# Kernel optimization log

Measured on AMD Instinct MI355X. Metric: run time of the kernel, lower is better.

The kernel has to match this reference:

```python
import jax, jax.numpy as jnp
import numpy as np


def setup_inputs() -> dict:
    key = jax.random.key(0)
    B, S, I, H, O = 32, 2048, 128, 512, 128
    ks = jax.random.split(key, 24)
    sc = 0.05
    d = {
        "x": jax.random.normal(ks[0], (B, S, I), jnp.float32),
        "h0": jnp.zeros((B, 2, H), jnp.float32),
        "l0_wxz": jax.random.normal(ks[1], (H, I)) * sc,
        "l0_bxz": jax.random.normal(ks[2], (H,)) * sc,
        "l0_whz": jax.random.normal(ks[3], (H, H)) * sc,
        "l0_wxr": jax.random.normal(ks[4], (H, I)) * sc,
        "l0_bxr": jax.random.normal(ks[5], (H,)) * sc,
        "l0_whr": jax.random.normal(ks[6], (H, H)) * sc,
        "l0_wxg": jax.random.normal(ks[7], (H, I)) * sc,
        "l0_bxg": jax.random.normal(ks[8], (H,)) * sc,
        "l0_whg": jax.random.normal(ks[9], (H, H)) * sc,
        "l1_wxz": jax.random.normal(ks[10], (H, H)) * sc,
        "l1_bxz": jax.random.normal(ks[11], (H,)) * sc,
        "l1_whz": jax.random.normal(ks[12], (H, H)) * sc,
        "l1_wxr": jax.random.normal(ks[13], (H, H)) * sc,
        "l1_bxr": jax.random.normal(ks[14], (H,)) * sc,
        "l1_whr": jax.random.normal(ks[15], (H, H)) * sc,
        "l1_wxg": jax.random.normal(ks[16], (H, H)) * sc,
        "l1_bxg": jax.random.normal(ks[17], (H,)) * sc,
        "l1_whg": jax.random.normal(ks[18], (H, H)) * sc,
        "wy": jax.random.normal(ks[19], (O, H)) * sc,
        "by": jax.random.normal(ks[20], (O,)) * sc,
    }
    return d


def _gru_cell(xt, h, wxz, bxz, whz, wxr, bxr, whr, wxg, bxg, whg):
    # z = sigmoid(Wxz x + bxz + Whz h); r = sigmoid(...); g = tanh(Wxg x + bxg + Whg (r*h))
    z = jax.nn.sigmoid(xt @ wxz.T + bxz + h @ whz.T)
    r = jax.nn.sigmoid(xt @ wxr.T + bxr + h @ whr.T)
    g = jnp.tanh(xt @ wxg.T + bxg + (r * h) @ whg.T)
    return z * h + (1.0 - z) * g


def reference(x, h0,
              l0_wxz, l0_bxz, l0_whz, l0_wxr, l0_bxr, l0_whr, l0_wxg, l0_bxg, l0_whg,
              l1_wxz, l1_bxz, l1_whz, l1_wxr, l1_bxr, l1_whr, l1_wxg, l1_bxg, l1_whg,
              wy, by):
    p0 = (l0_wxz, l0_bxz, l0_whz, l0_wxr, l0_bxr, l0_whr, l0_wxg, l0_bxg, l0_whg)
    p1 = (l1_wxz, l1_bxz, l1_whz, l1_wxr, l1_bxr, l1_whr, l1_wxg, l1_bxg, l1_whg)

    def step(carry, xt):  # xt: (B, I)
        h0_, h1_ = carry
        h0n = _gru_cell(xt, h0_, *p0)
        h1n = _gru_cell(h0n, h1_, *p1)
        y = h1n @ wy.T + by
        return (h0n, h1n), y

    xs = jnp.swapaxes(x, 0, 1)  # (S, B, I)
    init = (h0[:, 0, :], h0[:, 1, :])
    (hf0, hf1), ys = jax.lax.scan(step, init, xs)
    layer_output = jnp.swapaxes(ys, 0, 1)  # (B, S, O)
    hidden_state = jnp.stack([hf0, hf1], axis=1)  # (B, L, H)
    return layer_output, hidden_state
```

## Files before the change

kernel.cpp:

```cpp
#include <hip/hip_runtime.h>
#include <math.h>

typedef __bf16 bf16x8 __attribute__((ext_vector_type(8)));
typedef float f32x4 __attribute__((ext_vector_type(4)));
typedef unsigned short u16;
typedef unsigned int u32;
typedef unsigned long long u64;

#define MFMA16(a, b, c) __builtin_amdgcn_mfma_f32_16x16x32_bf16((a), (b), (c), 0, 0, 0)

namespace {
constexpr int kB = 32, kS = 2048, kI = 128, kH = 512, kO = 128;
constexpr int NC = 2;
constexpr int BPC = 16;
constexpr int L0WG = 16;
constexpr int WGC = 48;
constexpr int NT = 2 * kS + 3;
constexpr long LOUT = (long)kB * kS * kO;

constexpr size_t WS_FLG  = 0;
constexpr size_t WS_PUB0 = 8192;
constexpr size_t WS_PUB1 = WS_PUB0 + (size_t)NC * 2 * BPC * kH * 2;
constexpr size_t WS_PR0  = WS_PUB1 + (size_t)NC * 2 * BPC * kH * 2;
constexpr size_t WS_PR1  = WS_PR0  + (size_t)NC * 2 * BPC * kH * 2;
constexpr size_t WS_WTS  = WS_PR1  + (size_t)NC * 2 * BPC * kH * 2;

constexpr int W0H = 0;
constexpr int W0X = 786432;
constexpr int W1X = 983040;
constexpr int W1H = 1769472;
constexpr int WYO = 2555904;

constexpr int HP = 520;
constexpr int IP = 136;
}

__device__ __forceinline__ u16 f2bf(float f) {
  u32 x = __float_as_uint(f);
  return (u16)((x + 0x7fffu + ((x >> 16) & 1u)) >> 16);
}

__global__ void prep_kernel(const float* whz0, const float* whr0, const float* whg0,
                            const float* wxz0, const float* wxr0, const float* wxg0,
                            const float* wxz1, const float* wxr1, const float* wxg1,
                            const float* whz1, const float* whr1, const float* whg1,
                            const float* wy, const float* h0in, char* ws) {
  u16* wts = (u16*)(ws + WS_WTS);
  int gid = blockIdx.x * blockDim.x + threadIdx.x;
  int stride = gridDim.x * blockDim.x;
  for (int i = gid; i < 786432; i += stride) {
    int g = i >> 18, r = i & 262143;
    wts[W0H + i] = f2bf((g == 0 ? whz0 : g == 1 ? whr0 : whg0)[r]);
  }
  for (int i = gid; i < 196608; i += stride) {
    int g = i >> 16, r = i & 65535;
    wts[W0X + i] = f2bf((g == 0 ? wxz0 : g == 1 ? wxr0 : wxg0)[r]);
  }
  for (int i = gid; i < 786432; i += stride) {
    int g = i >> 18, r = i & 262143;
    wts[W1X + i] = f2bf((g == 0 ? wxz1 : g == 1 ? wxr1 : wxg1)[r]);
  }
  for (int i = gid; i < 786432; i += stride) {
    int g = i >> 18, r = i & 262143;
    wts[W1H + i] = f2bf((g == 0 ? whz1 : g == 1 ? whr1 : whg1)[r]);
  }
  for (int i = gid; i < 65536; i += stride) wts[WYO + i] = f2bf(wy[i]);

  u16* p0 = (u16*)(ws + WS_PUB0);
  u16* p1 = (u16*)(ws + WS_PUB1);
  for (int i = gid; i < NC * BPC * kH; i += stride) {
    int c = i / (BPC * kH), rem = i - c * (BPC * kH);
    int b = rem / kH, k = rem - b * kH;
    int bg = c * BPC + b;
    p0[(c * 2 + 1) * BPC * kH + rem] = f2bf(h0in[(size_t)bg * 2 * kH + k]);
    p1[(c * 2 + 1) * BPC * kH + rem] = f2bf(h0in[(size_t)bg * 2 * kH + kH + k]);
  }
  if (gid < 2048) ((u32*)(ws + WS_FLG))[gid] = 0u;
}

__device__ __forceinline__ void stage_c(u16* dst, const u16* src) {
  u64* s = (u64*)src;
  int t = threadIdx.x;
#pragma unroll
  for (int j = 0; j < 8; ++j) {
    int idx = j * 256 + t;
    u64 v = __hip_atomic_load(s + idx, __ATOMIC_RELAXED, __HIP_MEMORY_SCOPE_AGENT);
    int b = idx >> 7, i = idx & 127;
    *(u64*)(dst + b * HP + i * 4) = v;
  }
}
__device__ __forceinline__ void stage_c_half(u16* dst, const u16* src, int lt) {
  u64* s = (u64*)src;
#pragma unroll
  for (int j = 0; j < 16; ++j) {
    int idx = j * 128 + lt;
    u64 v = __hip_atomic_load(s + idx, __ATOMIC_RELAXED, __HIP_MEMORY_SCOPE_AGENT);
    int b = idx >> 7, i = idx & 127;
    *(u64*)(dst + b * HP + i * 4) = v;
  }
}

__device__ __forceinline__ void st_tile(float* base, f32x4 c, int q, int li) {
#pragma unroll
  for (int r = 0; r < 4; ++r) base[(q * 4 + r) * 17 + li] = c[r];
}

__device__ __forceinline__ void pub2(u16* base, int off, float v0, float v1) {
  u32 pk = (u32)f2bf(v0) | ((u32)f2bf(v1) << 16);
  __hip_atomic_store((u32*)(base + off), pk, __ATOMIC_RELAXED, __HIP_MEMORY_SCOPE_AGENT);
}

__device__ __forceinline__ float sigm(float x) { return 1.f / (1.f + __expf(-x)); }
__device__ __forceinline__ float tanh_f(float x) {
  float te = __expf(-2.f * fabsf(x));
  return __builtin_copysignf((1.f - te) / (1.f + te), x);
}

__device__ __forceinline__ void cbar(u32* flags, int wid, u32 target) {
  __syncthreads();
  if (threadIdx.x == 0)
    __hip_atomic_store(&flags[wid * 16], target, __ATOMIC_RELAXED, __HIP_MEMORY_SCOPE_AGENT);
  if (threadIdx.x < WGC) {
    while (__hip_atomic_load(&flags[threadIdx.x * 16], __ATOMIC_RELAXED,
                             __HIP_MEMORY_SCOPE_AGENT) < target)
      __builtin_amdgcn_s_sleep(1);
  }
  __syncthreads();
}

__global__ __launch_bounds__(256, 1)
void gru_kernel(const float* __restrict__ xg, const float* __restrict__ h0in,
                const float* __restrict__ bxz0, const float* __restrict__ bxr0,
                const float* __restrict__ bxg0, const float* __restrict__ bxz1,
                const float* __restrict__ bxr1, const float* __restrict__ bxg1,
                const float* __restrict__ byv, float* __restrict__ out, char* ws) {
  const int cl = blockIdx.x / WGC;
  const int wid = blockIdx.x - cl * WGC;
  const bool isL0 = wid < L0WG;
  const int w0 = wid, w1 = wid - L0WG;
  const int tid = threadIdx.x;
  const int lane = tid & 63, wv = tid >> 6;
  const int q = lane >> 4, li = lane & 15;
  const int kh = wv & 1;
  const int nt = wv >> 1;
  const bool xside = wv < 2;

  u16* pub0 = (u16*)(ws + WS_PUB0) + (size_t)cl * 2 * BPC * kH;
  u16* pub1 = (u16*)(ws + WS_PUB1) + (size_t)cl * 2 * BPC * kH;
  u16* pr0  = (u16*)(ws + WS_PR0)  + (size_t)cl * 2 * BPC * kH;
  u16* pr1  = (u16*)(ws + WS_PR1)  + (size_t)cl * 2 * BPC * kH;
  const u16* wts = (const u16*)(ws + WS_WTS);
  u32* flags = (u32*)(ws + WS_FLG) + (size_t)cl * 1024;

  __shared__ __align__(16) char smem[57216];
  u16* h0buf = (u16*)smem;
  u16* h1buf = (u16*)(smem + 16640);
  u16* xbuf  = (u16*)(smem + 16640);
  u16* rhbuf = (u16*)smem;
  float* spA = (float*)(smem + 33280);
  float* spB = (float*)(smem + 33280);
  float* ypA = (float*)(smem + 55040);

  bf16x8 wA[3][8];
  bf16x8 wE[8];
  if (isL0) {
    const int ci = w0 * 32 + nt * 16 + li;
#pragma unroll
    for (int g = 0; g < 3; ++g)
#pragma unroll
      for (int s = 0; s < 8; ++s)
        wA[g][s] = *(const bf16x8*)(wts + W0H + ((size_t)(g * kH + ci) * kH + kh * 256 + q * 8 + s * 32));
#pragma unroll
    for (int g = 0; g < 3; ++g)
#pragma unroll
      for (int s = 0; s < 2; ++s)
        wE[g * 2 + s] = *(const bf16x8*)(wts + W0X + ((size_t)(g * kH + ci) * kI + kh * 64 + q * 8 + s * 32));
  } else {
    const int ci = w1 * 16 + li;
    const int base = xside ? W1X : W1H;
#pragma unroll
    for (int g = 0; g < 3; ++g)
#pragma unroll
      for (int s = 0; s < 8; ++s)
        wA[g][s] = *(const bf16x8*)(wts + base + ((size_t)(g * kH + ci) * kH + kh * 256 + q * 8 + s * 32));
    if (!xside && w1 < 8) {
#pragma unroll
      for (int s = 0; s < 8; ++s)
        wE[s] = *(const bf16x8*)(wts + WYO + ((size_t)ci * kH + kh * 256 + q * 8 + s * 32));
    }
  }

  float2 bz2 = {0.f, 0.f}, br2 = {0.f, 0.f}, bg2 = {0.f, 0.f};
  float by_r = 0.f;
  float hm0r = 0.f, hm1r = 0.f;
  float zA0 = 0.f, zA1 = 0.f, gA0 = 0.f, gA1 = 0.f;
  if (isL0) {
    const int c0i = (tid & 15) * 2, bq = tid >> 4;
    bz2 = *(const float2*)(bxz0 + w0 * 32 + c0i);
    br2 = *(const float2*)(bxr0 + w0 * 32 + c0i);
    bg2 = *(const float2*)(bxg0 + w0 * 32 + c0i);
    const float* hp = h0in + (size_t)(cl * 16 + bq) * 2 * kH + w0 * 32 + c0i;
    hm0r = hp[0]; hm1r = hp[1];
  } else {
    const int c0i = (tid & 7) * 2, bq = tid >> 3;
    bz2 = *(const float2*)(bxz1 + w1 * 16 + c0i);
    br2 = *(const float2*)(bxr1 + w1 * 16 + c0i);
    bg2 = *(const float2*)(bxg1 + w1 * 16 + c0i);
    if (bq < 16) {
      const float* hp = h0in + (size_t)(cl * 16 + bq) * 2 * kH + kH + w1 * 16 + c0i;
      hm0r = hp[0]; hm1r = hp[1];
    }
    if (w1 < 8) by_r = byv[w1 * 16 + (tid & 15)];
  }

  for (int tk = 0; tk < NT; ++tk) {
    const bool ev = (tk & 1) == 0;
    const int t = tk >> 1;
    const int u = t - 1;
    const bool l0A = isL0 && ev && t < kS;
    const bool l0B = isL0 && !ev && t < kS;
    const bool l1A = !isL0 && ev && t >= 1 && t <= kS;
    const bool l1B = !isL0 && !ev && t >= 1 && t <= kS;
    const bool stH1 = !isL0 && ev && t >= 1 && t <= kS + 1;
    const bool yAct = !isL0 && ev && w1 < 8 && t >= 2 && t <= kS + 1;

    if (l0A) {
      stage_c(h0buf, pub0 + ((t - 1) & 1) * BPC * kH);
      int b = tid >> 4, i0 = (tid & 15) * 8;
      const float* xr = xg + ((size_t)(cl * 16 + b) * kS + t) * kI + i0;
      float4 v0 = *(const float4*)xr;
      float4 v1 = *(const float4*)(xr + 4);
      int4 pk;
      pk.x = (int)((u32)f2bf(v0.x) | ((u32)f2bf(v0.y) << 16));
      pk.y = (int)((u32)f2bf(v0.z) | ((u32)f2bf(v0.w) << 16));
      pk.z = (int)((u32)f2bf(v1.x) | ((u32)f2bf(v1.y) << 16));
      pk.w = (int)((u32)f2bf(v1.z) | ((u32)f2bf(v1.w) << 16));
      *(int4*)(xbuf + b * IP + i0) = pk;
    }
    if (!isL0 && ev) {
      if (tid < 128) {
        if (l1A) stage_c_half(h0buf, pub0 + (u & 1) * BPC * kH, tid);
      } else {
        if (stH1) stage_c_half(h1buf, pub1 + ((u - 1) & 1) * BPC * kH, tid - 128);
      }
    }
    if (l0B) stage_c(rhbuf, pr0 + (t & 1) * BPC * kH);
    if (l1B) stage_c(rhbuf, pr1 + (u & 1) * BPC * kH);
    __syncthreads();

    if (l0A) {
      f32x4 hz = {0.f, 0.f, 0.f, 0.f}, hr = hz, xz = hz, xr2 = hz, xg2 = hz;
      const u16* ap = h0buf + li * HP + kh * 256 + q * 8;
#pragma unroll
      for (int s = 0; s < 8; ++s) {
        bf16x8 a = *(const bf16x8*)(ap + s * 32);
        hz = MFMA16(a, wA[0][s], hz);
        hr = MFMA16(a, wA[1][s], hr);
      }
      const u16* xp = xbuf + li * IP + kh * 64 + q * 8;
#pragma unroll
      for (int s = 0; s < 2; ++s) {
        bf16x8 a = *(const bf16x8*)(xp + s * 32);
        xz  = MFMA16(a, wE[0 + s], xz);
        xr2 = MFMA16(a, wE[2 + s], xr2);
        xg2 = MFMA16(a, wE[4 + s], xg2);
      }
      st_tile(spA + ((0 * 2 + nt) * 2 + kh) * 272, hz, q, li);
      st_tile(spA + ((1 * 2 + nt) * 2 + kh) * 272, hr, q, li);
      st_tile(spA + ((2 * 2 + nt) * 2 + kh) * 272, xz, q, li);
      st_tile(spA + ((3 * 2 + nt) * 2 + kh) * 272, xr2, q, li);
      st_tile(spA + ((4 * 2 + nt) * 2 + kh) * 272, xg2, q, li);
    } else if (!isL0 && ev) {
      if (xside) {
        if (l1A) {
          f32x4 cz = {0.f, 0.f, 0.f, 0.f}, cr = cz, cg = cz;
          const u16* ap = h0buf + li * HP + kh * 256 + q * 8;
#pragma unroll
          for (int s = 0; s < 8; ++s) {
            bf16x8 a = *(const bf16x8*)(ap + s * 32);
            cz = MFMA16(a, wA[0][s], cz);
            cr = MFMA16(a, wA[1][s], cr);
            cg = MFMA16(a, wA[2][s], cg);
          }
          st_tile(spA + (2 * 2 + kh) * 272, cz, q, li);
          st_tile(spA + (3 * 2 + kh) * 272, cr, q, li);
          st_tile(spA + (4 * 2 + kh) * 272, cg, q, li);
        }
      } else {
        const bool rec = t >= 1 && t <= kS;
        const bool ym = (w1 < 8) && t >= 2 && t <= kS + 1;
        if (rec || ym) {
          f32x4 cz = {0.f, 0.f, 0.f, 0.f}, cr = cz, cy = cz;
          const u16* ap = h1buf + li * HP + kh * 256 + q * 8;
#pragma unroll
          for (int s = 0; s < 8; ++s) {
            bf16x8 a = *(const bf16x8*)(ap + s * 32);
            if (rec) {
              cz = MFMA16(a, wA[0][s], cz);
              cr = MFMA16(a, wA[1][s], cr);
            }
            if (ym) cy = MFMA16(a, wE[s], cy);
          }
          if (rec) {
            st_tile(spA + (0 * 2 + kh) * 272, cz, q, li);
            st_tile(spA + (1 * 2 + kh) * 272, cr, q, li);
          }
          if (ym) st_tile(ypA + kh * 272, cy, q, li);
        }
      }
    } else if (l0B) {
      f32x4 cg = {0.f, 0.f, 0.f, 0.f};
      const u16* ap = rhbuf + li * HP + kh * 256 + q * 8;
#pragma unroll
      for (int s = 0; s < 8; ++s)
        cg = MFMA16(*(const bf16x8*)(ap + s * 32), wA[2][s], cg);
      st_tile(spB + (nt * 2 + kh) * 272, cg, q, li);
    } else if (l1B && !xside) {
      f32x4 cg = {0.f, 0.f, 0.f, 0.f};
      const u16* ap = rhbuf + li * HP + kh * 256 + q * 8;
#pragma unroll
      for (int s = 0; s < 8; ++s)
        cg = MFMA16(*(const bf16x8*)(ap + s * 32), wA[2][s], cg);
      st_tile(spB + kh * 272, cg, q, li);
    }
    __syncthreads();

    if (l0A) {
      const int cp = tid & 15, b = tid >> 4;
      const int c0 = cp * 2, n2 = c0 >> 4, cc = c0 & 15, o = b * 17 + cc;
      float hz0 = spA[((0*2+n2)*2+0)*272 + o] + spA[((0*2+n2)*2+1)*272 + o];
      float hz1 = spA[((0*2+n2)*2+0)*272 + o+1] + spA[((0*2+n2)*2+1)*272 + o+1];
      float hr0 = spA[((1*2+n2)*2+0)*272 + o] + spA[((1*2+n2)*2+1)*272 + o];
      float hr1 = spA[((1*2+n2)*2+0)*272 + o+1] + spA[((1*2+n2)*2+1)*272 + o+1];
      float xz0 = spA[((2*2+n2)*2+0)*272 + o] + spA[((2*2+n2)*2+1)*272 + o];
      float xz1 = spA[((2*2+n2)*2+0)*272 + o+1] + spA[((2*2+n2)*2+1)*272 + o+1];
      float xr0 = spA[((3*2+n2)*2+0)*272 + o] + spA[((3*2+n2)*2+1)*272 + o];
      float xr1 = spA[((3*2+n2)*2+0)*272 + o+1] + spA[((3*2+n2)*2+1)*272 + o+1];
      float xg0 = spA[((4*2+n2)*2+0)*272 + o] + spA[((4*2+n2)*2+1)*272 + o];
      float xg1 = spA[((4*2+n2)*2+0)*272 + o+1] + spA[((4*2+n2)*2+1)*272 + o+1];
      zA0 = sigm(hz0 + xz0 + bz2.x);
      zA1 = sigm(hz1 + xz1 + bz2.y);
      float r0 = sigm(hr0 + xr0 + br2.x);
      float r1 = sigm(hr1 + xr1 + br2.y);
      gA0 = xg0 + bg2.x;
      gA1 = xg1 + bg2.y;
      pub2(pr0 + (t & 1) * BPC * kH, b * kH + w0 * 32 + c0, r0 * hm0r, r1 * hm1r);
    }
    if (l1A && tid < 128) {
      const int cp = tid & 7, b = tid >> 3;
      const int c0 = cp * 2, o = b * 17 + c0;
      float hz0 = spA[(0*2+0)*272 + o] + spA[(0*2+1)*272 + o];
      float hz1 = spA[(0*2+0)*272 + o+1] + spA[(0*2+1)*272 + o+1];
      float hr0 = spA[(1*2+0)*272 + o] + spA[(1*2+1)*272 + o];
      float hr1 = spA[(1*2+0)*272 + o+1] + spA[(1*2+1)*272 + o+1];
      float xz0 = spA[(2*2+0)*272 + o] + spA[(2*2+1)*272 + o];
      float xz1 = spA[(2*2+0)*272 + o+1] + spA[(2*2+1)*272 + o+1];
      float xr0 = spA[(3*2+0)*272 + o] + spA[(3*2+1)*272 + o];
      float xr1 = spA[(3*2+0)*272 + o+1] + spA[(3*2+1)*272 + o+1];
      float xg0 = spA[(4*2+0)*272 + o] + spA[(4*2+1)*272 + o];
      float xg1 = spA[(4*2+0)*272 + o+1] + spA[(4*2+1)*272 + o+1];
      zA0 = sigm(hz0 + xz0 + bz2.x);
      zA1 = sigm(hz1 + xz1 + bz2.y);
      float r0 = sigm(hr0 + xr0 + br2.x);
      float r1 = sigm(hr1 + xr1 + br2.y);
      gA0 = xg0 + bg2.x;
      gA1 = xg1 + bg2.y;
      pub2(pr1 + (u & 1) * BPC * kH, b * kH + w1 * 16 + c0, r0 * hm0r, r1 * hm1r);
    }
    if (yAct) {
      const int c = tid & 15, b = tid >> 4;
      float y = ypA[b * 17 + c] + ypA[272 + b * 17 + c] + by_r;
      out[((size_t)(cl * 16 + b) * kS + (t - 2)) * kO + w1 * 16 + c] = y;
    }
    if (l0B) {
      const int cp = tid & 15, b = tid >> 4;
      const int c0 = cp * 2, n2 = c0 >> 4, cc = c0 & 15, o = b * 17 + cc;
      float gh0 = spB[(n2*2+0)*272 + o] + spB[(n2*2+1)*272 + o];
      float gh1 = spB[(n2*2+0)*272 + o+1] + spB[(n2*2+1)*272 + o+1];
      float g0 = tanh_f(gA0 + gh0), g1 = tanh_f(gA1 + gh1);
      float hn0 = zA0 * hm0r + (1.f - zA0) * g0;
      float hn1 = zA1 * hm1r + (1.f - zA1) * g1;
      hm0r = hn0; hm1r = hn1;
      pub2(pub0 + (t & 1) * BPC * kH, b * kH + w0 * 32 + c0, hn0, hn1);
      if (t == kS - 1) {
        float* op = out + LOUT + (size_t)(cl * 16 + b) * 2 * kH + w0 * 32 + c0;
        op[0] = hn0; op[1] = hn1;
      }
    }
    if (l1B && tid < 128) {
      const int cp = tid & 7, b = tid >> 3;
      const int c0 = cp * 2, o = b * 17 + c0;
      float gh0 = spB[0 * 272 + o] + spB[1 * 272 + o];
      float gh1 = spB[0 * 272 + o+1] + spB[1 * 272 + o+1];
      float g0 = tanh_f(gA0 + gh0), g1 = tanh_f(gA1 + gh1);
      float hn0 = zA0 * hm0r + (1.f - zA0) * g0;
      float hn1 = zA1 * hm1r + (1.f - zA1) * g1;
      hm0r = hn0; hm1r = hn1;
      pub2(pub1 + (u & 1) * BPC * kH, b * kH + w1 * 16 + c0, hn0, hn1);
      if (u == kS - 1) {
        float* op = out + LOUT + (size_t)(cl * 16 + b) * 2 * kH + kH + w1 * 16 + c0;
        op[0] = hn0; op[1] = hn1;
      }
    }

    if (tk != NT - 1) cbar(flags, wid, (u32)(tk + 1));
  }
}

extern "C" void kernel_launch(void* const* d_in, const int* in_sizes, int n_in,
                              void* d_out, int out_size, void* d_ws, size_t ws_size,
                              hipStream_t stream) {
  (void)in_sizes; (void)n_in; (void)out_size; (void)ws_size;
  const float* x      = (const float*)d_in[0];
  const float* h0     = (const float*)d_in[1];
  const float* l0_wxz = (const float*)d_in[2];
  const float* l0_bxz = (const float*)d_in[3];
  const float* l0_whz = (const float*)d_in[4];
  const float* l0_wxr = (const float*)d_in[5];
  const float* l0_bxr = (const float*)d_in[6];
  const float* l0_whr = (const float*)d_in[7];
  const float* l0_wxg = (const float*)d_in[8];
  const float* l0_bxg = (const float*)d_in[9];
  const float* l0_whg = (const float*)d_in[10];
  const float* l1_wxz = (const float*)d_in[11];
  const float* l1_bxz = (const float*)d_in[12];
  const float* l1_whz = (const float*)d_in[13];
  const float* l1_wxr = (const float*)d_in[14];
  const float* l1_bxr = (const float*)d_in[15];
  const float* l1_whr = (const float*)d_in[16];
  const float* l1_wxg = (const float*)d_in[17];
  const float* l1_bxg = (const float*)d_in[18];
  const float* l1_whg = (const float*)d_in[19];
  const float* wy     = (const float*)d_in[20];
  const float* by     = (const float*)d_in[21];
  float* out = (float*)d_out;
  char* ws = (char*)d_ws;

  prep_kernel<<<512, 256, 0, stream>>>(l0_whz, l0_whr, l0_whg, l0_wxz, l0_wxr, l0_wxg,
                                       l1_wxz, l1_wxr, l1_wxg, l1_whz, l1_whr, l1_whg,
                                       wy, h0, ws);
  gru_kernel<<<NC * WGC, 256, 0, stream>>>(x, h0, l0_bxz, l0_bxr, l0_bxg,
                                           l1_bxz, l1_bxr, l1_bxg, by, out, ws);
}
```

Before: 19.86 ms.

## Replace per-step cluster barrier with poison-value dataflow sync and 4-slot ring buffers

```diff
diff --git a/kernel.cpp b/kernel.cpp
--- a/kernel.cpp
+++ b/kernel.cpp
@@ -1,5 +1,4 @@
 #include <hip/hip_runtime.h>
-#include <math.h>
 
 typedef __bf16 bf16x8 __attribute__((ext_vector_type(8)));
 typedef float f32x4 __attribute__((ext_vector_type(4)));
@@ -15,15 +14,18 @@
 constexpr int BPC = 16;
 constexpr int L0WG = 16;
 constexpr int WGC = 48;
+constexpr int NSLOT = 4;
 constexpr int NT = 2 * kS + 3;
 constexpr long LOUT = (long)kB * kS * kO;
+constexpr u32 POISON = 0xFFFFFFFFu;
 
 constexpr size_t WS_FLG  = 0;
 constexpr size_t WS_PUB0 = 8192;
-constexpr size_t WS_PUB1 = WS_PUB0 + (size_t)NC * 2 * BPC * kH * 2;
-constexpr size_t WS_PR0  = WS_PUB1 + (size_t)NC * 2 * BPC * kH * 2;
-constexpr size_t WS_PR1  = WS_PR0  + (size_t)NC * 2 * BPC * kH * 2;
-constexpr size_t WS_WTS  = WS_PR1  + (size_t)NC * 2 * BPC * kH * 2;
+constexpr size_t BUFSZ   = (size_t)NC * NSLOT * BPC * kH * 2;
+constexpr size_t WS_PUB1 = WS_PUB0 + BUFSZ;
+constexpr size_t WS_PR0  = WS_PUB1 + BUFSZ;
+constexpr size_t WS_PR1  = WS_PR0 + BUFSZ;
+constexpr size_t WS_WTS  = WS_PR1 + BUFSZ;
 
 constexpr int W0H = 0;
 constexpr int W0X = 786432;
@@ -31,13 +33,51 @@
 constexpr int W1H = 1769472;
 constexpr int WYO = 2555904;
 
-constexpr int HP = 520;
-constexpr int IP = 136;
+constexpr int CSLOT = BPC * kH;
+constexpr int CBUF  = NSLOT * CSLOT;
 }
 
 __device__ __forceinline__ u16 f2bf(float f) {
   u32 x = __float_as_uint(f);
   return (u16)((x + 0x7fffu + ((x >> 16) & 1u)) >> 16);
+}
+
+__device__ __forceinline__ u64 ld64a(const u64* p) {
+  return __hip_atomic_load((u64*)p, __ATOMIC_RELAXED, __HIP_MEMORY_SCOPE_AGENT);
+}
+__device__ __forceinline__ u32 ld32a(const u32* p) {
+  return __hip_atomic_load((u32*)p, __ATOMIC_RELAXED, __HIP_MEMORY_SCOPE_AGENT);
+}
+__device__ __forceinline__ bool bad(u64 v) {
+  return ((u32)v == POISON) | ((u32)(v >> 32) == POISON);
+}
+
+struct Frags {
+  u64 v[16];
+  const u64* p;
+  __device__ __forceinline__ void issue(const u16* base) {
+    p = (const u64*)base;
+#pragma unroll
+    for (int s = 0; s < 8; ++s) {
+      v[2 * s]     = ld64a(p + s * 8);
+      v[2 * s + 1] = ld64a(p + s * 8 + 1);
+    }
+  }
+  __device__ __forceinline__ bf16x8 get(int s) {
+    u64 a = v[2 * s], b = v[2 * s + 1];
+    while (bad(a)) a = ld64a(p + s * 8);
+    while (bad(b)) b = ld64a(p + s * 8 + 1);
+    union { u64 d[2]; bf16x8 f; } u_;
+    u_.d[0] = a; u_.d[1] = b;
+    return u_.f;
+  }
+};
+
+__device__ __forceinline__ bf16x8 pack8(float4 a, float4 b) {
+  union { u16 s[8]; bf16x8 v; } u_;
+  u_.s[0] = f2bf(a.x); u_.s[1] = f2bf(a.y); u_.s[2] = f2bf(a.z); u_.s[3] = f2bf(a.w);
+  u_.s[4] = f2bf(b.x); u_.s[5] = f2bf(b.y); u_.s[6] = f2bf(b.z); u_.s[7] = f2bf(b.w);
+  return u_.v;
 }
 
 __global__ void prep_kernel(const float* whz0, const float* whr0, const float* whg0,
@@ -66,38 +106,26 @@
   }
   for (int i = gid; i < 65536; i += stride) wts[WYO + i] = f2bf(wy[i]);
 
+  u32* r0 = (u32*)(ws + WS_PR0);
+  u32* r1 = (u32*)(ws + WS_PR1);
+  u32* b0 = (u32*)(ws + WS_PUB0);
+  u32* b1 = (u32*)(ws + WS_PUB1);
+  constexpr int NW = (int)(BUFSZ / 4);
+  for (int i = gid; i < NW; i += stride) { r0[i] = POISON; r1[i] = POISON; }
+  for (int i = gid; i < NW; i += stride) {
+    int s = (i >> 12) & 3;
+    if (s != 3) { b0[i] = POISON; b1[i] = POISON; }
+  }
   u16* p0 = (u16*)(ws + WS_PUB0);
   u16* p1 = (u16*)(ws + WS_PUB1);
   for (int i = gid; i < NC * BPC * kH; i += stride) {
     int c = i / (BPC * kH), rem = i - c * (BPC * kH);
     int b = rem / kH, k = rem - b * kH;
     int bg = c * BPC + b;
-    p0[(c * 2 + 1) * BPC * kH + rem] = f2bf(h0in[(size_t)bg * 2 * kH + k]);
-    p1[(c * 2 + 1) * BPC * kH + rem] = f2bf(h0in[(size_t)bg * 2 * kH + kH + k]);
+    p0[c * CBUF + 3 * CSLOT + rem] = f2bf(h0in[(size_t)bg * 2 * kH + k]);
+    p1[c * CBUF + 3 * CSLOT + rem] = f2bf(h0in[(size_t)bg * 2 * kH + kH + k]);
   }
   if (gid < 2048) ((u32*)(ws + WS_FLG))[gid] = 0u;
-}
-
-__device__ __forceinline__ void stage_c(u16* dst, const u16* src) {
-  u64* s = (u64*)src;
-  int t = threadIdx.x;
-#pragma unroll
-  for (int j = 0; j < 8; ++j) {
-    int idx = j * 256 + t;
-    u64 v = __hip_atomic_load(s + idx, __ATOMIC_RELAXED, __HIP_MEMORY_SCOPE_AGENT);
-    int b = idx >> 7, i = idx & 127;
-    *(u64*)(dst + b * HP + i * 4) = v;
-  }
-}
-__device__ __forceinline__ void stage_c_half(u16* dst, const u16* src, int lt) {
-  u64* s = (u64*)src;
-#pragma unroll
-  for (int j = 0; j < 16; ++j) {
-    int idx = j * 128 + lt;
-    u64 v = __hip_atomic_load(s + idx, __ATOMIC_RELAXED, __HIP_MEMORY_SCOPE_AGENT);
-    int b = idx >> 7, i = idx & 127;
-    *(u64*)(dst + b * HP + i * 4) = v;
-  }
 }
 
 __device__ __forceinline__ void st_tile(float* base, f32x4 c, int q, int li) {
@@ -108,24 +136,15 @@
 __device__ __forceinline__ void pub2(u16* base, int off, float v0, float v1) {
   u32 pk = (u32)f2bf(v0) | ((u32)f2bf(v1) << 16);
   __hip_atomic_store((u32*)(base + off), pk, __ATOMIC_RELAXED, __HIP_MEMORY_SCOPE_AGENT);
+}
+__device__ __forceinline__ void poison2(u16* base, int off) {
+  __hip_atomic_store((u32*)(base + off), POISON, __ATOMIC_RELAXED, __HIP_MEMORY_SCOPE_AGENT);
 }
 
 __device__ __forceinline__ float sigm(float x) { return 1.f / (1.f + __expf(-x)); }
 __device__ __forceinline__ float tanh_f(float x) {
   float te = __expf(-2.f * fabsf(x));
   return __builtin_copysignf((1.f - te) / (1.f + te), x);
-}
-
-__device__ __forceinline__ void cbar(u32* flags, int wid, u32 target) {
-  __syncthreads();
-  if (threadIdx.x == 0)
-    __hip_atomic_store(&flags[wid * 16], target, __ATOMIC_RELAXED, __HIP_MEMORY_SCOPE_AGENT);
-  if (threadIdx.x < WGC) {
-    while (__hip_atomic_load(&flags[threadIdx.x * 16], __ATOMIC_RELAXED,
-                             __HIP_MEMORY_SCOPE_AGENT) < target)
-      __builtin_amdgcn_s_sleep(1);
-  }
-  __syncthreads();
 }
 
 __global__ __launch_bounds__(256, 1)
@@ -145,21 +164,17 @@
   const int nt = wv >> 1;
   const bool xside = wv < 2;
 
-  u16* pub0 = (u16*)(ws + WS_PUB0) + (size_t)cl * 2 * BPC * kH;
-  u16* pub1 = (u16*)(ws + WS_PUB1) + (size_t)cl * 2 * BPC * kH;
-  u16* pr0  = (u16*)(ws + WS_PR0)  + (size_t)cl * 2 * BPC * kH;
-  u16* pr1  = (u16*)(ws + WS_PR1)  + (size_t)cl * 2 * BPC * kH;
+  u16* pub0 = (u16*)(ws + WS_PUB0) + (size_t)cl * CBUF;
+  u16* pub1 = (u16*)(ws + WS_PUB1) + (size_t)cl * CBUF;
+  u16* pr0  = (u16*)(ws + WS_PR0)  + (size_t)cl * CBUF;
+  u16* pr1  = (u16*)(ws + WS_PR1)  + (size_t)cl * CBUF;
   const u16* wts = (const u16*)(ws + WS_WTS);
   u32* flags = (u32*)(ws + WS_FLG) + (size_t)cl * 1024;
 
-  __shared__ __align__(16) char smem[57216];
-  u16* h0buf = (u16*)smem;
-  u16* h1buf = (u16*)(smem + 16640);
-  u16* xbuf  = (u16*)(smem + 16640);
-  u16* rhbuf = (u16*)smem;
-  float* spA = (float*)(smem + 33280);
-  float* spB = (float*)(smem + 33280);
-  float* ypA = (float*)(smem + 55040);
+  __shared__ __align__(16) float smem[5984];
+  float* spA = smem;
+  float* spB = smem;
+  float* ypA = smem + 5440;
 
   bf16x8 wA[3][8];
   bf16x8 wE[8];
@@ -221,49 +236,38 @@
     const bool l0B = isL0 && !ev && t < kS;
     const bool l1A = !isL0 && ev && t >= 1 && t <= kS;
     const bool l1B = !isL0 && !ev && t >= 1 && t <= kS;
-    const bool stH1 = !isL0 && ev && t >= 1 && t <= kS + 1;
     const bool yAct = !isL0 && ev && w1 < 8 && t >= 2 && t <= kS + 1;
 
+    u32 myfl = 0xFFFFFFFFu;
+    if (lane < WGC) myfl = ld32a(flags + lane * 16);
+    const u32 need = (tk >= 2) ? (u32)(tk - 2) : 0u;
+
     if (l0A) {
-      stage_c(h0buf, pub0 + ((t - 1) & 1) * BPC * kH);
-      int b = tid >> 4, i0 = (tid & 15) * 8;
-      const float* xr = xg + ((size_t)(cl * 16 + b) * kS + t) * kI + i0;
-      float4 v0 = *(const float4*)xr;
-      float4 v1 = *(const float4*)(xr + 4);
-      int4 pk;
-      pk.x = (int)((u32)f2bf(v0.x) | ((u32)f2bf(v0.y) << 16));
-      pk.y = (int)((u32)f2bf(v0.z) | ((u32)f2bf(v0.w) << 16));
-      pk.z = (int)((u32)f2bf(v1.x) | ((u32)f2bf(v1.y) << 16));
-      pk.w = (int)((u32)f2bf(v1.z) | ((u32)f2bf(v1.w) << 16));
-      *(int4*)(xbuf + b * IP + i0) = pk;
-    }
-    if (!isL0 && ev) {
-      if (tid < 128) {
-        if (l1A) stage_c_half(h0buf, pub0 + (u & 1) * BPC * kH, tid);
-      } else {
-        if (stH1) stage_c_half(h1buf, pub1 + ((u - 1) & 1) * BPC * kH, tid - 128);
-      }
-    }
-    if (l0B) stage_c(rhbuf, pr0 + (t & 1) * BPC * kH);
-    if (l1B) stage_c(rhbuf, pr1 + (u & 1) * BPC * kH);
-    __syncthreads();
-
-    if (l0A) {
+      Frags F;
+      F.issue(pub0 + ((t + 3) & 3) * CSLOT + li * kH + kh * 256 + q * 8);
+      const float* xr = xg + ((size_t)(cl * 16 + li) * kS + t) * kI + kh * 64 + q * 8;
+      float4 xv0 = *(const float4*)xr;
+      float4 xv1 = *(const float4*)(xr + 4);
+      float4 xv2 = *(const float4*)(xr + 32);
+      float4 xv3 = *(const float4*)(xr + 36);
       f32x4 hz = {0.f, 0.f, 0.f, 0.f}, hr = hz, xz = hz, xr2 = hz, xg2 = hz;
-      const u16* ap = h0buf + li * HP + kh * 256 + q * 8;
 #pragma unroll
       for (int s = 0; s < 8; ++s) {
-        bf16x8 a = *(const bf16x8*)(ap + s * 32);
+        bf16x8 a = F.get(s);
         hz = MFMA16(a, wA[0][s], hz);
         hr = MFMA16(a, wA[1][s], hr);
       }
-      const u16* xp = xbuf + li * IP + kh * 64 + q * 8;
-#pragma unroll
-      for (int s = 0; s < 2; ++s) {
-        bf16x8 a = *(const bf16x8*)(xp + s * 32);
-        xz  = MFMA16(a, wE[0 + s], xz);
-        xr2 = MFMA16(a, wE[2 + s], xr2);
-        xg2 = MFMA16(a, wE[4 + s], xg2);
+      {
+        bf16x8 a = pack8(xv0, xv1);
+        xz  = MFMA16(a, wE[0], xz);
+        xr2 = MFMA16(a, wE[2], xr2);
+        xg2 = MFMA16(a, wE[4], xg2);
+      }
+      {
+        bf16x8 a = pack8(xv2, xv3);
+        xz  = MFMA16(a, wE[1], xz);
+        xr2 = MFMA16(a, wE[3], xr2);
+        xg2 = MFMA16(a, wE[5], xg2);
       }
       st_tile(spA + ((0 * 2 + nt) * 2 + kh) * 272, hz, q, li);
       st_tile(spA + ((1 * 2 + nt) * 2 + kh) * 272, hr, q, li);
@@ -273,11 +277,12 @@
     } else if (!isL0 && ev) {
       if (xside) {
         if (l1A) {
+          Frags F;
+          F.issue(pub0 + (u & 3) * CSLOT + li * kH + kh * 256 + q * 8);
           f32x4 cz = {0.f, 0.f, 0.f, 0.f}, cr = cz, cg = cz;
-          const u16* ap = h0buf + li * HP + kh * 256 + q * 8;
 #pragma unroll
           for (int s = 0; s < 8; ++s) {
-            bf16x8 a = *(const bf16x8*)(ap + s * 32);
+            bf16x8 a = F.get(s);
             cz = MFMA16(a, wA[0][s], cz);
             cr = MFMA16(a, wA[1][s], cr);
             cg = MFMA16(a, wA[2][s], cg);
@@ -290,11 +295,12 @@
         const bool rec = t >= 1 && t <= kS;
         const bool ym = (w1 < 8) && t >= 2 && t <= kS + 1;
         if (rec || ym) {
+          Frags F;
+          F.issue(pub1 + ((t + 2) & 3) * CSLOT + li * kH + kh * 256 + q * 8);
           f32x4 cz = {0.f, 0.f, 0.f, 0.f}, cr = cz, cy = cz;
-          const u16* ap = h1buf + li * HP + kh * 256 + q * 8;
 #pragma unroll
           for (int s = 0; s < 8; ++s) {
-            bf16x8 a = *(const bf16x8*)(ap + s * 32);
+            bf16x8 a = F.get(s);
             if (rec) {
               cz = MFMA16(a, wA[0][s], cz);
               cr = MFMA16(a, wA[1][s], cr);
@@ -309,21 +315,25 @@
         }
       }
     } else if (l0B) {
+      Frags F;
+      F.issue(pr0 + (t & 3) * CSLOT + li * kH + kh * 256 + q * 8);
       f32x4 cg = {0.f, 0.f, 0.f, 0.f};
-      const u16* ap = rhbuf + li * HP + kh * 256 + q * 8;
-#pragma unroll
-      for (int s = 0; s < 8; ++s)
-        cg = MFMA16(*(const bf16x8*)(ap + s * 32), wA[2][s], cg);
+#pragma unroll
+      for (int s = 0; s < 8; ++s) cg = MFMA16(F.get(s), wA[2][s], cg);
       st_tile(spB + (nt * 2 + kh) * 272, cg, q, li);
     } else if (l1B && !xside) {
+      Frags F;
+      F.issue(pr1 + (u & 3) * CSLOT + li * kH + kh * 256 + q * 8);
       f32x4 cg = {0.f, 0.f, 0.f, 0.f};
-      const u16* ap = rhbuf + li * HP + kh * 256 + q * 8;
-#pragma unroll
-      for (int s = 0; s < 8; ++s)
-        cg = MFMA16(*(const bf16x8*)(ap + s * 32), wA[2][s], cg);
+#pragma unroll
+      for (int s = 0; s < 8; ++s) cg = MFMA16(F.get(s), wA[2][s], cg);
       st_tile(spB + kh * 272, cg, q, li);
     }
     __syncthreads();
+
+    while (__any((int)(myfl < need))) {
+      if (lane < WGC) myfl = ld32a(flags + lane * 16);
+    }
 
     if (l0A) {
       const int cp = tid & 15, b = tid >> 4;
@@ -340,11 +350,13 @@
       float xg1 = spA[((4*2+n2)*2+0)*272 + o+1] + spA[((4*2+n2)*2+1)*272 + o+1];
       zA0 = sigm(hz0 + xz0 + bz2.x);
       zA1 = sigm(hz1 + xz1 + bz2.y);
-      float r0 = sigm(hr0 + xr0 + br2.x);
-      float r1 = sigm(hr1 + xr1 + br2.y);
+      float r0v = sigm(hr0 + xr0 + br2.x);
+      float r1v = sigm(hr1 + xr1 + br2.y);
       gA0 = xg0 + bg2.x;
       gA1 = xg1 + bg2.y;
-      pub2(pr0 + (t & 1) * BPC * kH, b * kH + w0 * 32 + c0, r0 * hm0r, r1 * hm1r);
+      const int off = b * kH + w0 * 32 + c0;
+      pub2(pr0 + (t & 3) * CSLOT, off, r0v * hm0r, r1v * hm1r);
+      poison2(pr0 + ((t + 2) & 3) * CSLOT, off);
     }
     if (l1A && tid < 128) {
       const int cp = tid & 7, b = tid >> 3;
@@ -361,11 +373,13 @@
       float xg1 = spA[(4*2+0)*272 + o+1] + spA[(4*2+1)*272 + o+1];
       zA0 = sigm(hz0 + xz0 + bz2.x);
       zA1 = sigm(hz1 + xz1 + bz2.y);
-      float r0 = sigm(hr0 + xr0 + br2.x);
-      float r1 = sigm(hr1 + xr1 + br2.y);
+      float r0v = sigm(hr0 + xr0 + br2.x);
+      float r1v = sigm(hr1 + xr1 + br2.y);
       gA0 = xg0 + bg2.x;
       gA1 = xg1 + bg2.y;
-      pub2(pr1 + (u & 1) * BPC * kH, b * kH + w1 * 16 + c0, r0 * hm0r, r1 * hm1r);
+      const int off = b * kH + w1 * 16 + c0;
+      pub2(pr1 + (u & 3) * CSLOT, off, r0v * hm0r, r1v * hm1r);
+      poison2(pr1 + ((u + 2) & 3) * CSLOT, off);
     }
     if (yAct) {
       const int c = tid & 15, b = tid >> 4;
@@ -381,7 +395,9 @@
       float hn0 = zA0 * hm0r + (1.f - zA0) * g0;
       float hn1 = zA1 * hm1r + (1.f - zA1) * g1;
       hm0r = hn0; hm1r = hn1;
-      pub2(pub0 + (t & 1) * BPC * kH, b * kH + w0 * 32 + c0, hn0, hn1);
+      const int off = b * kH + w0 * 32 + c0;
+      pub2(pub0 + (t & 3) * CSLOT, off, hn0, hn1);
+      poison2(pub0 + ((t + 2) & 3) * CSLOT, off);
       if (t == kS - 1) {
         float* op = out + LOUT + (size_t)(cl * 16 + b) * 2 * kH + w0 * 32 + c0;
         op[0] = hn0; op[1] = hn1;
@@ -396,14 +412,19 @@
       float hn0 = zA0 * hm0r + (1.f - zA0) * g0;
       float hn1 = zA1 * hm1r + (1.f - zA1) * g1;
       hm0r = hn0; hm1r = hn1;
-      pub2(pub1 + (u & 1) * BPC * kH, b * kH + w1 * 16 + c0, hn0, hn1);
+      const int off = b * kH + w1 * 16 + c0;
+      pub2(pub1 + (u & 3) * CSLOT, off, hn0, hn1);
+      poison2(pub1 + ((u + 2) & 3) * CSLOT, off);
       if (u == kS - 1) {
         float* op = out + LOUT + (size_t)(cl * 16 + b) * 2 * kH + kH + w1 * 16 + c0;
         op[0] = hn0; op[1] = hn1;
       }
     }
 
-    if (tk != NT - 1) cbar(flags, wid, (u32)(tk + 1));
+    __syncthreads();
+    if (tid == 0 && tk != NT - 1)
+      __hip_atomic_store(flags + wid * 16, (u32)(tk + 1), __ATOMIC_RELAXED,
+                         __HIP_MEMORY_SCOPE_AGENT);
   }
 }
 
```

After: 16.51 ms. 16.8% less time.
